# Optimization experiments

Hardware: AMD Instinct MI355X
Metric: run time of the kernel (lower is better)

Reference implementation:

```python
import jax, jax.numpy as jnp
import numpy as np

N = 50000   # nodes
E = 200000  # edges per relation
R = 4       # relations
IN = 128
HID = 32
H = 4
OUT = 32


def setup_inputs() -> dict:
    key = jax.random.key(0)
    ks = jax.random.split(key, 32)
    w = lambda k, shape: jax.random.normal(k, shape, jnp.float32) * 0.05
    inp = {
        "x": jax.random.normal(ks[0], (N, IN), jnp.float32),
        "edge_src": jax.random.randint(ks[1], (R, E), 0, N, dtype=jnp.int32),
        "edge_dst": jax.random.randint(ks[2], (R, E), 0, N, dtype=jnp.int32),
    }
    # (d_in, heads*d_out, d_out) per layer: flatten, flatten, mean-over-heads
    dims = [(IN, H * HID, HID), (H * HID, H * HID, HID), (H * HID, H * OUT, OUT)]
    i = 3
    for l, (din, dout, d) in enumerate(dims):
        inp[f"Wsrc{l}"] = w(ks[i], (R, din, dout)); i += 1
        inp[f"bsrc{l}"] = w(ks[i], (R, dout)); i += 1
        inp[f"Wdst{l}"] = w(ks[i], (R, din, dout)); i += 1
        inp[f"bdst{l}"] = w(ks[i], (R, dout)); i += 1
        inp[f"attn{l}"] = w(ks[i], (R, H, d)); i += 1
    return inp


def rel_gatv2(h, src, dst, Ws, bs, Wd, bd, att):
    """DGL GATv2Conv for one relation: gather, leaky-relu score, edge softmax, scatter-sum."""
    n = h.shape[0]
    heads, d = att.shape
    fs = (h @ Ws + bs).reshape(n, heads, d)   # [N,H,D]
    fd = (h @ Wd + bd).reshape(n, heads, d)
    e = jax.nn.leaky_relu(fs[src] + fd[dst], 0.2)        # [E,H,D]
    score = jnp.einsum('ehd,hd->eh', e, att)             # [E,H]
    # numerically stable edge softmax segmented by destination node
    m = jax.lax.stop_gradient(jax.ops.segment_max(score, dst, num_segments=n))
    m = jnp.where(jnp.isfinite(m), m, 0.0)               # zero-in-degree guard
    ex = jnp.exp(score - m[dst])
    den = jax.ops.segment_sum(ex, dst, num_segments=n)
    a = ex / jnp.maximum(den[dst], 1e-16)                # [E,H]
    return jax.ops.segment_sum(a[:, :, None] * fs[src], dst, num_segments=n)  # [N,H,D]


def gat_layer(h, edge_src, edge_dst, Ws, bs, Wd, bd, att, mean_heads):
    out = None
    for r in range(Ws.shape[0]):  # small fixed relation count; HeteroGraphConv sums
        o = rel_gatv2(h, edge_src[r], edge_dst[r], Ws[r], bs[r], Wd[r], bd[r], att[r])
        out = o if out is None else out + o
    if mean_heads:                # last_layer_flag: mean over heads
        return out.mean(axis=1)
    return out.reshape(h.shape[0], -1)  # flatten heads


def reference(x, edge_src, edge_dst,
              Wsrc0, bsrc0, Wdst0, bdst0, attn0,
              Wsrc1, bsrc1, Wdst1, bdst1, attn1,
              Wsrc2, bsrc2, Wdst2, bdst2, attn2):
    h = gat_layer(x, edge_src, edge_dst, Wsrc0, bsrc0, Wdst0, bdst0, attn0, False)
    h = gat_layer(h, edge_src, edge_dst, Wsrc1, bsrc1, Wdst1, bdst1, attn1, False)
    h = gat_layer(h, edge_src, edge_dst, Wsrc2, bsrc2, Wdst2, bdst2, attn2, True)
    return h  # [N, OUT]
```

## Files before the change

kernel.cpp:

```cpp
#include <hip/hip_runtime.h>
#include <math.h>

#define FF 128
#define G0F 1024
#define GG 2048

typedef _Float16 half2v __attribute__((ext_vector_type(2)));
typedef _Float16 f16x8  __attribute__((ext_vector_type(8)));
typedef __fp16   fp16x2 __attribute__((ext_vector_type(2)));
typedef __attribute__((ext_vector_type(4))) float f4v;

__device__ __forceinline__ half2v u2h(unsigned u) {
    union { unsigned u; half2v h; } c; c.u = u; return c.h;
}
__device__ __forceinline__ unsigned h2u(half2v h) {
    union { unsigned u; half2v h; } c; c.h = h; return c.u;
}
__device__ __forceinline__ unsigned short f2h(float f) {
    _Float16 h = (_Float16)f;
    unsigned short u; __builtin_memcpy(&u, &h, 2); return u;
}
__device__ __forceinline__ half2v pk2h(float e) {
    union { fp16x2 p; half2v h; } c;
    c.p = __builtin_amdgcn_cvt_pkrtz(e, e);
    return c.h;
}
__device__ __forceinline__ float dot2(half2v a, half2v b, float c) {
#if __has_builtin(__builtin_amdgcn_fdot2)
    union { half2v h; fp16x2 p; } ca, cb;
    ca.h = a; cb.h = b;
    return __builtin_amdgcn_fdot2(ca.p, cb.p, c, false);
#else
    return c + (float)a.x * (float)b.x + (float)a.y * (float)b.y;
#endif
}
__device__ __forceinline__ half2v shfladd_h(half2v v, int mask) {
    return v + u2h(__shfl_xor(h2u(v), mask));
}
__device__ __forceinline__ int swz16(int row, int chunk) {
    return row * 256 + (((chunk ^ row) & 15) << 4);
}


__global__ __launch_bounds__(256) void pack0(
    const float* __restrict__ W0s_, const float* __restrict__ W0d_,
    unsigned short* __restrict__ Wp,
    const float* __restrict__ a0, const float* __restrict__ a1,
    const float* __restrict__ a2, unsigned* __restrict__ attH)
{
    int b = blockIdx.x;
    const int tid = threadIdx.x;
    if (b < 512) {
        const int t = b * 256 + tid;
        const int r   = t >> 15;
        const int mat = (t >> 14) & 1;
        const int idx = t & 16383;
        const int k = idx >> 7, nn = idx & 127;
        const float* W = mat ? W0d_ : W0s_;
        const float v = W[((size_t)r * FF + k) * FF + nn];
        const int nb = nn >> 4, lo = nn & 15;
        const int ks = k >> 5, quad = (k >> 3) & 3, j = k & 7;
        const int lane = quad * 16 + lo;
        const size_t o = ((((((size_t)r * 2 + mat) * 8 + nb) * 4 + ks) * 64 + lane) * 8) + j;
        Wp[o] = f2h(v);
        return;
    }
    b -= 512;
    const int t = b * 256 + tid;
    if (t >= 768) return;
    const int l = t >> 8, rest = t & 255;
    const float* a = (l == 0) ? a0 : (l == 1) ? a1 : a2;
    const float2 v = ((const float2*)a)[rest];
    half2v h = {(_Float16)v.x, (_Float16)v.y};
    attH[t] = h2u(h);
}

__global__ __launch_bounds__(256, 4) void fused2(
    const int* __restrict__ esrc_all, const int* __restrict__ edst_all,
    int* __restrict__ rec, int* __restrict__ ovf,
    int totalE, int ne, int n, int CB,
    const float* __restrict__ x,
    const unsigned short* __restrict__ Wp,
    const float* __restrict__ bs0, const float* __restrict__ bd0,
    unsigned short* __restrict__ fs_all, unsigned short* __restrict__ fd_all,
    int nrb,
    const float* __restrict__ W1s_, const float* __restrict__ W1d_,
    const float* __restrict__ W2s_, const float* __restrict__ W2d_,
    unsigned short* __restrict__ Wp_full)
{
    __shared__ char lsA[4096];
    __shared__ char lsC[8192];

    int b = blockIdx.x;
    const int tid = threadIdx.x;
    const int L = n << 2;

    if (b < CB) {
        const int t0 = b * 1024 + tid;
        #pragma unroll
        for (int k = 0; k < 4; ++k) {
            const int i = t0 + k * 256;
            if (i < totalE) {
                const int r = i / ne;
                const int rd = r * n + edst_all[i];
                const int src = esrc_all[i];
                const int idx = atomicAdd(&rec[(size_t)rd * 16], 1);
                if (idx < 15)      rec[(size_t)rd * 16 + 1 + idx] = src;
                else if (idx < 32) ovf[(size_t)(idx - 15) * L + rd] = src;
            }
        }
        return;
    }
    b -= CB;

    if (b < G0F) {
        const int wave = tid >> 6, lane = tid & 63;
        const int r = b & 3;
        const int half = wave & 1;
        const int mat  = wave >> 1;
        const int lo = lane & 15, quad = lane >> 4;

        const unsigned short* Wr = Wp + (size_t)r * 2 * FF * FF;
        const float* bp = mat ? bd0 : bs0;
        unsigned short* fs = fs_all + (size_t)r * n * FF;
        unsigned short* fd = fd_all + (size_t)r * n * FF;

        f16x8 B[4][4];
        #pragma unroll
        for (int nbi = 0; nbi < 4; ++nbi)
            #pragma unroll
            for (int ks = 0; ks < 4; ++ks) {
                const int nb = half * 4 + nbi;
                B[nbi][ks] = *(const f16x8*)
                    &Wr[(((((size_t)mat * 8 + nb) * 4 + ks) * 64 + lane) * 8)];
            }

        float bias[4];
        #pragma unroll
        for (int nbi = 0; nbi < 4; ++nbi)
            bias[nbi] = bp[r * FF + (half * 4 + nbi) * 16 + lo];

        const int srow = tid >> 4, schunk = tid & 15;
        const int stride = G0F >> 2;
        for (int rb = b >> 2; rb < nrb; rb += stride) {
            const int row0 = rb * 16;
            {
                const float* xs = &x[(size_t)row0 * FF + tid * 8];
                const float4 p0 = *(const float4*)&xs[0];
                const float4 p1 = *(const float4*)&xs[4];
                f16x8 v;
                v[0] = (_Float16)p0.x; v[1] = (_Float16)p0.y;
                v[2] = (_Float16)p0.z; v[3] = (_Float16)p0.w;
                v[4] = (_Float16)p1.x; v[5] = (_Float16)p1.y;
                v[6] = (_Float16)p1.z; v[7] = (_Float16)p1.w;
                *(f16x8*)&lsA[swz16(srow, schunk)] = v;
            }
            __syncthreads();

            f16x8 A[4];
            #pragma unroll
            for (int ks = 0; ks < 4; ++ks)
                A[ks] = *(const f16x8*)&lsA[swz16(lo, ks * 4 + quad)];

            f4v c[4];
            #pragma unroll
            for (int nbi = 0; nbi < 4; ++nbi)
                c[nbi] = (f4v){bias[nbi], bias[nbi], bias[nbi], bias[nbi]};

            #pragma unroll
            for (int ks = 0; ks < 4; ++ks)
                #pragma unroll
                for (int nbi = 0; nbi < 4; ++nbi)
                    c[nbi] = __builtin_amdgcn_mfma_f32_16x16x32_f16(
                        A[ks], B[nbi][ks], c[nbi], 0, 0, 0);

            #pragma unroll
            for (int nbi = 0; nbi < 4; ++nbi)
                #pragma unroll
                for (int i = 0; i < 4; ++i) {
                    const int row = quad * 4 + i;
                    const int cb  = ((half * 4 + nbi) * 16 + lo) * 2;
                    *(unsigned short*)&lsC[mat * 4096 + swz16(row, cb >> 4) + (cb & 15)]
                        = f2h(c[nbi][i]);
                }
            __syncthreads();

            #pragma unroll
            for (int p = 0; p < 2; ++p) {
                const int unit = p * 256 + tid;
                const int m    = unit >> 8;
                const int row  = (unit >> 4) & 15;
                const int ch   = unit & 15;
                const uint4 d = *(const uint4*)&lsC[m * 4096 + swz16(row, ch)];
                unsigned short* out = m ? fd : fs;
                *(uint4*)&out[(size_t)(row0 + row) * FF + ch * 8] = d;
            }
            __syncthreads();
        }
        return;
    }
    b -= G0F;

    const int t = b * 256 + tid;
    if (t >= 2 * 4 * 2 * FF * FF) return;
    const int l    = 1 + (t >> 17);
    const int rest = t & 131071;
    const int r    = rest >> 15;
    const int mat  = (rest >> 14) & 1;
    const int idx  = rest & 16383;
    const int k = idx >> 7, nn = idx & 127;
    const float* W = (l == 1) ? (mat ? W1d_ : W1s_)
                              : (mat ? W2d_ : W2s_);
    const float v = W[((size_t)r * FF + k) * FF + nn];
    const int nb = nn >> 4, lo = nn & 15;
    const int ks = k >> 5, quad = (k >> 3) & 3, j = k & 7;
    const int lane = quad * 16 + lo;
    const size_t o = (((((((size_t)l * 4 + r) * 2 + mat) * 8 + nb) * 4 + ks) * 64 + lane) * 8) + j;
    Wp_full[o] = f2h(v);
}

__global__ __launch_bounds__(256, 4) void mfma_gemm(
    const unsigned short* __restrict__ hb,
    const unsigned short* __restrict__ Wp,
    const float* __restrict__ bs_all,
    const float* __restrict__ bd_all,
    unsigned short* __restrict__ fs_all,
    unsigned short* __restrict__ fd_all,
    int nrb, int n)
{
    __shared__ char lsA[4096];
    __shared__ char lsC[8192];

    const int tid = threadIdx.x;
    const int wave = tid >> 6, lane = tid & 63;
    const int r = blockIdx.x & 3;
    const int half = wave & 1;
    const int mat  = wave >> 1;
    const int lo = lane & 15, quad = lane >> 4;

    const unsigned short* Wr = Wp + (size_t)r * 2 * FF * FF;
    const float* bp = mat ? bd_all : bs_all;
    unsigned short* fs = fs_all + (size_t)r * n * FF;
    unsigned short* fd = fd_all + (size_t)r * n * FF;

    f16x8 B[4][4];
    #pragma unroll
    for (int nbi = 0; nbi < 4; ++nbi)
        #pragma unroll
        for (int ks = 0; ks < 4; ++ks) {
            const int nb = half * 4 + nbi;
            B[nbi][ks] = *(const f16x8*)
                &Wr[(((((size_t)mat * 8 + nb) * 4 + ks) * 64 + lane) * 8)];
        }

    float bias[4];
    #pragma unroll
    for (int nbi = 0; nbi < 4; ++nbi)
        bias[nbi] = bp[r * FF + (half * 4 + nbi) * 16 + lo];

    const int srow = tid >> 4, schunk = tid & 15;
    const int stride = gridDim.x >> 2;
    for (int rb = blockIdx.x >> 2; rb < nrb; rb += stride) {
        const int row0 = rb * 16;
        {
            const uint4 g = *(const uint4*)&hb[(size_t)row0 * FF + tid * 8];
            *(uint4*)&lsA[swz16(srow, schunk)] = g;
        }
        __syncthreads();

        f16x8 A[4];
        #pragma unroll
        for (int ks = 0; ks < 4; ++ks)
            A[ks] = *(const f16x8*)&lsA[swz16(lo, ks * 4 + quad)];

        f4v c[4];
        #pragma unroll
        for (int nbi = 0; nbi < 4; ++nbi)
            c[nbi] = (f4v){bias[nbi], bias[nbi], bias[nbi], bias[nbi]};

        #pragma unroll
        for (int ks = 0; ks < 4; ++ks)
            #pragma unroll
            for (int nbi = 0; nbi < 4; ++nbi)
                c[nbi] = __builtin_amdgcn_mfma_f32_16x16x32_f16(
                    A[ks], B[nbi][ks], c[nbi], 0, 0, 0);

        #pragma unroll
        for (int nbi = 0; nbi < 4; ++nbi)
            #pragma unroll
            for (int i = 0; i < 4; ++i) {
                const int row = quad * 4 + i;
                const int cb  = ((half * 4 + nbi) * 16 + lo) * 2;
                *(unsigned short*)&lsC[mat * 4096 + swz16(row, cb >> 4) + (cb & 15)]
                    = f2h(c[nbi][i]);
            }
        __syncthreads();

        #pragma unroll
        for (int p = 0; p < 2; ++p) {
            const int unit = p * 256 + tid;
            const int m    = unit >> 8;
            const int row  = (unit >> 4) & 15;
            const int ch   = unit & 15;
            const uint4 d = *(const uint4*)&lsC[m * 4096 + swz16(row, ch)];
            unsigned short* out = m ? fd : fs;
            *(uint4*)&out[(size_t)(row0 + row) * FF + ch * 8] = d;
        }
        __syncthreads();
    }
}

__device__ __forceinline__ void edge4(
    uint4 g, bool ok, const half2v* fdv, const half2v* atv,
    float& den, half2v* acc)
{
    const half2v C02 = {(_Float16)0.2f, (_Float16)0.2f};
    half2v f[4] = {u2h(g.x), u2h(g.y), u2h(g.z), u2h(g.w)};
    float v = 0.f;
    #pragma unroll
    for (int i = 0; i < 4; ++i) {
        const half2v z = f[i] + fdv[i];
        const half2v l = __builtin_elementwise_max(z, z * C02);
        v = dot2(l, atv[i], v);
    }
    v += __shfl_xor(v, 2);
    v += __shfl_xor(v, 1);
    const float e = ok ? __expf(v) : 0.f;
    den += e;
    const half2v eh = pk2h(e);
    #pragma unroll
    for (int i = 0; i < 4; ++i) acc[i] += eh * f[i];
}

__global__ __launch_bounds__(256) void aggregate(
    const int* __restrict__ rec,
    const int* __restrict__ ovf,
    const unsigned* __restrict__ fs_all,
    const unsigned* __restrict__ fd_all,
    const unsigned* __restrict__ att_h,
    unsigned* __restrict__ out_h,
    float* __restrict__ out_f32,
    int n)
{
    const int node = blockIdx.x * 4 + (threadIdx.x >> 6);
    if (node >= n) return;
    const int lane = threadIdx.x & 63;
    const int quarter = lane >> 4;
    const int q = lane & 15;
    const int fo = 4 * q;
    const int L = n << 2;

    int m[4], i0[4], i1[4];
    #pragma unroll
    for (int r = 0; r < 4; ++r) {
        const int rd = r * n + node;
        const int* rp = &rec[(size_t)rd * 16];
        m[r]  = rp[0];
        i0[r] = rp[1 + quarter];
        i1[r] = rp[5 + quarter];
    }

    half2v val[4];
    #pragma unroll
    for (int i = 0; i < 4; ++i) val[i] = (half2v){(_Float16)0.f, (_Float16)0.f};

    #pragma unroll
    for (int rp2 = 0; rp2 < 2; ++rp2) {
        const int ra = 2 * rp2, rb = 2 * rp2 + 1;
        const int rdA = ra * n + node;
        const int rdB = rb * n + node;
        const int mA = m[ra], mB = m[rb];
        const unsigned* fsuA = fs_all + (size_t)ra * n * 64;
        const unsigned* fsuB = fs_all + (size_t)rb * n * 64;

        const uint4 ufdA = *(const uint4*)&fd_all[(size_t)rdA * 64 + fo];
        const uint4 ufdB = *(const uint4*)&fd_all[(size_t)rdB * 64 + fo];
        const uint4 uatA = *(const uint4*)&att_h[ra * 64 + fo];
        const uint4 uatB = *(const uint4*)&att_h[rb * 64 + fo];

        const bool okA0 = quarter < mA, okA1 = 4 + quarter < mA;
        const bool okB0 = quarter < mB, okB1 = 4 + quarter < mB;
        int iA0 = okA0 ? i0[ra] : 0;
        int iB0 = okB0 ? i0[rb] : 0;
        int iA1 = okA1 ? i1[ra] : 0;
        int iB1 = okB1 ? i1[rb] : 0;
        const uint4 gA0 = *(const uint4*)&fsuA[(size_t)iA0 * 64 + fo];
        const uint4 gB0 = *(const uint4*)&fsuB[(size_t)iB0 * 64 + fo];
        const uint4 gA1 = *(const uint4*)&fsuA[(size_t)iA1 * 64 + fo];
        const uint4 gB1 = *(const uint4*)&fsuB[(size_t)iB1 * 64 + fo];

        half2v fdvA[4] = {u2h(ufdA.x), u2h(ufdA.y), u2h(ufdA.z), u2h(ufdA.w)};
        half2v atvA[4] = {u2h(uatA.x), u2h(uatA.y), u2h(uatA.z), u2h(uatA.w)};
        half2v fdvB[4] = {u2h(ufdB.x), u2h(ufdB.y), u2h(ufdB.z), u2h(ufdB.w)};
        half2v atvB[4] = {u2h(uatB.x), u2h(uatB.y), u2h(uatB.z), u2h(uatB.w)};

        float denA = 0.f, denB = 0.f;
        half2v accA[4], accB[4];
        #pragma unroll
        for (int i = 0; i < 4; ++i) {
            accA[i] = (half2v){(_Float16)0.f, (_Float16)0.f};
            accB[i] = (half2v){(_Float16)0.f, (_Float16)0.f};
        }

        edge4(gA0, okA0, fdvA, atvA, denA, accA);
        edge4(gB0, okB0, fdvB, atvB, denB, accB);
        if (mA > 4) edge4(gA1, okA1, fdvA, atvA, denA, accA);
        if (mB > 4) edge4(gB1, okB1, fdvB, atvB, denB, accB);

        if (mA > 8) {
            for (int p = 8; p < mA; p += 4) {
                const int ei = p + quarter;
                const bool ok = ei < mA;
                const int eic = ei < 31 ? ei : 31;
                int s = (eic < 15) ? rec[(size_t)rdA * 16 + 1 + eic]
                                   : ovf[(size_t)(eic - 15) * L + rdA];
                s = ok ? s : 0;
                const uint4 g = *(const uint4*)&fsuA[(size_t)s * 64 + fo];
                edge4(g, ok, fdvA, atvA, denA, accA);
            }
        }
        if (mB > 8) {
            for (int p = 8; p < mB; p += 4) {
                const int ei = p + quarter;
                const bool ok = ei < mB;
                const int eic = ei < 31 ? ei : 31;
                int s = (eic < 15) ? rec[(size_t)rdB * 16 + 1 + eic]
                                   : ovf[(size_t)(eic - 15) * L + rdB];
                s = ok ? s : 0;
                const uint4 g = *(const uint4*)&fsuB[(size_t)s * 64 + fo];
                edge4(g, ok, fdvB, atvB, denB, accB);
            }
        }

        if (mA) {
            denA += __shfl_xor(denA, 16);
            denA += __shfl_xor(denA, 32);
            const half2v ih = pk2h(__builtin_amdgcn_rcpf(denA));
            #pragma unroll
            for (int i = 0; i < 4; ++i) val[i] += accA[i] * ih;
        }
        if (mB) {
            denB += __shfl_xor(denB, 16);
            denB += __shfl_xor(denB, 32);
            const half2v ih = pk2h(__builtin_amdgcn_rcpf(denB));
            #pragma unroll
            for (int i = 0; i < 4; ++i) val[i] += accB[i] * ih;
        }
    }

    #pragma unroll
    for (int i = 0; i < 4; ++i) {
        val[i] = shfladd_h(val[i], 16);
        val[i] = shfladd_h(val[i], 32);
    }

    if (out_f32) {
        #pragma unroll
        for (int i = 0; i < 4; ++i) {
            val[i] = shfladd_h(val[i], 4);
            val[i] = shfladd_h(val[i], 8);
        }
        if (lane < 4) {
            float* o = &out_f32[(size_t)node * 32 + 8 * lane];
            *(float4*)&o[0] = make_float4(0.25f * (float)val[0].x, 0.25f * (float)val[0].y,
                                          0.25f * (float)val[1].x, 0.25f * (float)val[1].y);
            *(float4*)&o[4] = make_float4(0.25f * (float)val[2].x, 0.25f * (float)val[2].y,
                                          0.25f * (float)val[3].x, 0.25f * (float)val[3].y);
        }
    } else {
        if (lane < 16) {
            uint4 o;
            o.x = h2u(val[0]); o.y = h2u(val[1]);
            o.z = h2u(val[2]); o.w = h2u(val[3]);
            *(uint4*)&out_h[(size_t)node * 64 + fo] = o;
        }
    }
}

extern "C" void kernel_launch(void* const* d_in, const int* in_sizes, int n_in,
                              void* d_out, int out_size, void* d_ws, size_t ws_size,
                              hipStream_t stream)
{
    const int n  = in_sizes[0] / FF;
    const int R  = 4;
    const int ne = in_sizes[1] / R;
    const int totalE = R * ne;
    const int L  = R * n;
    const int nrb = (n + 15) / 16;

    const float* x    = (const float*)d_in[0];
    const int*   esrc = (const int*)d_in[1];
    const int*   edst = (const int*)d_in[2];

    char* p = (char*)d_ws;
    auto carve = [&p](size_t bytes) { char* q = p; p += (bytes + 255) & ~(size_t)255; return q; };
    unsigned*       hbA    = (unsigned*)      carve((size_t)n * 64 * 4);
    unsigned*       hbB    = (unsigned*)      carve((size_t)n * 64 * 4);
    unsigned short* fs_all = (unsigned short*)carve((size_t)R * n * FF * 2);
    unsigned short* fd_all = (unsigned short*)carve((size_t)R * n * FF * 2);
    unsigned short* Wp     = (unsigned short*)carve((size_t)3 * R * 2 * FF * FF * 2);
    unsigned*       attH   = (unsigned*)      carve((size_t)3 * R * 64 * 4);
    int*            rec    = (int*)           carve((size_t)L * 16 * 4);
    int*            ovf    = (int*)           carve((size_t)17 * L * 4);

    (void)hipMemsetAsync(rec, 0, (size_t)L * 16 * sizeof(int), stream);

    pack0<<<515, 256, 0, stream>>>(
        (const float*)d_in[3], (const float*)d_in[5], Wp,
        (const float*)d_in[7], (const float*)d_in[12], (const float*)d_in[17],
        attH);

    const int CB = (totalE + 1023) / 1024;
    fused2<<<CB + G0F + 1024, 256, 0, stream>>>(
        esrc, edst, rec, ovf, totalE, ne, n, CB,
        x, Wp,
        (const float*)d_in[4], (const float*)d_in[6],
        fs_all, fd_all, nrb,
        (const float*)d_in[8],  (const float*)d_in[10],
        (const float*)d_in[13], (const float*)d_in[15],
        Wp);

    unsigned* bufs[3] = {hbA, hbB, nullptr};
    for (int l = 0; l < 3; ++l) {
        if (l > 0) {
            const float* bsrc = (const float*)d_in[3 + 5 * l + 1];
            const float* bdst = (const float*)d_in[3 + 5 * l + 3];
            mfma_gemm<<<GG, 256, 0, stream>>>(
                (const unsigned short*)bufs[l - 1],
                Wp + (size_t)l * R * 2 * FF * FF,
                bsrc, bdst, fs_all, fd_all, nrb, n);
        }
        const int last = (l == 2);
        aggregate<<<(n + 3) / 4, 256, 0, stream>>>(
            rec, ovf,
            (const unsigned*)fs_all, (const unsigned*)fd_all,
            attH + (size_t)l * R * 64,
            last ? nullptr : bufs[l],
            last ? (float*)d_out : nullptr, n);
    }
}
```

Measured before the change: 376.2 us.

## Bucket edges by destination block, then build adjacency records in shared memory

```diff
diff --git a/kernel.cpp b/kernel.cpp
--- a/kernel.cpp
+++ b/kernel.cpp
@@ -4,6 +4,8 @@
 #define FF 128
 #define G0F 1024
 #define GG 2048
+#define BSH 8
+#define CAPB 256
 
 typedef _Float16 half2v __attribute__((ext_vector_type(2)));
 typedef _Float16 f16x8  __attribute__((ext_vector_type(8)));
@@ -75,10 +77,10 @@
     attH[t] = h2u(h);
 }
 
-__global__ __launch_bounds__(256, 4) void fused2(
+__global__ __launch_bounds__(256, 4) void fused3(
     const int* __restrict__ esrc_all, const int* __restrict__ edst_all,
-    int* __restrict__ rec, int* __restrict__ ovf,
-    int totalE, int ne, int n, int CB,
+    int* __restrict__ bcur, unsigned* __restrict__ bbuf,
+    int totalE, int ne, int n, int NB, int CB2,
     const float* __restrict__ x,
     const unsigned short* __restrict__ Wp,
     const float* __restrict__ bs0, const float* __restrict__ bd0,
@@ -93,9 +95,9 @@
 
     int b = blockIdx.x;
     const int tid = threadIdx.x;
-    const int L = n << 2;
-
-    if (b < CB) {
+
+    if (b < CB2) {
+        const int part = b & 7;
         const int t0 = b * 1024 + tid;
         #pragma unroll
         for (int k = 0; k < 4; ++k) {
@@ -104,14 +106,17 @@
                 const int r = i / ne;
                 const int rd = r * n + edst_all[i];
                 const int src = esrc_all[i];
-                const int idx = atomicAdd(&rec[(size_t)rd * 16], 1);
-                if (idx < 15)      rec[(size_t)rd * 16 + 1 + idx] = src;
-                else if (idx < 32) ovf[(size_t)(idx - 15) * L + rd] = src;
+                const int bkt = rd >> BSH;
+                const int reg = part * NB + bkt;
+                const int pos = atomicAdd(&bcur[reg << 4], 1);
+                if (pos < CAPB)
+                    bbuf[((size_t)reg << 8) + pos] =
+                        ((unsigned)(rd & 255) << 16) | (unsigned)src;
             }
         }
         return;
     }
-    b -= CB;
+    b -= CB2;
 
     if (b < G0F) {
         const int wave = tid >> 6, lane = tid & 63;
@@ -219,6 +224,49 @@
     Wp_full[o] = f2h(v);
 }
 
+__global__ __launch_bounds__(256) void p3build(
+    const int* __restrict__ bcur, const unsigned* __restrict__ bbuf,
+    int* __restrict__ rec, int* __restrict__ ovf, int NB, int L)
+{
+    __shared__ int lrec[256 * 17];
+    const int b = blockIdx.x;
+    const int tid = threadIdx.x;
+
+    #pragma unroll
+    for (int k = 0; k < 17; ++k) lrec[k * 256 + tid] = 0;
+    __syncthreads();
+
+    const int rd0 = b << BSH;
+    for (int part = 0; part < 8; ++part) {
+        const int reg = part * NB + b;
+        int c = bcur[reg << 4];
+        c = c < CAPB ? c : CAPB;
+        const unsigned* seg = &bbuf[(size_t)reg << 8];
+        for (int e = tid; e < c; e += 256) {
+            const unsigned v = seg[e];
+            const int rdL = v >> 16;
+            const int src = (int)(v & 0xFFFFu);
+            const int idx = atomicAdd(&lrec[rdL * 17], 1);
+            if (idx < 15)      lrec[rdL * 17 + 1 + idx] = src;
+            else if (idx < 32) ovf[(size_t)(idx - 15) * L + rd0 + rdL] = src;
+        }
+    }
+    __syncthreads();
+
+    if (rd0 + tid < L) {
+        int* out = &rec[(size_t)(rd0 + tid) * 16];
+        #pragma unroll
+        for (int w = 0; w < 4; ++w) {
+            int4 d;
+            d.x = lrec[tid * 17 + w * 4 + 0];
+            d.y = lrec[tid * 17 + w * 4 + 1];
+            d.z = lrec[tid * 17 + w * 4 + 2];
+            d.w = lrec[tid * 17 + w * 4 + 3];
+            *(int4*)&out[w * 4] = d;
+        }
+    }
+}
+
 __global__ __launch_bounds__(256, 4) void mfma_gemm(
     const unsigned short* __restrict__ hb,
     const unsigned short* __restrict__ Wp,
@@ -487,6 +535,7 @@
     const int totalE = R * ne;
     const int L  = R * n;
     const int nrb = (n + 15) / 16;
+    const int NB = (L + 255) >> BSH;
 
     const float* x    = (const float*)d_in[0];
     const int*   esrc = (const int*)d_in[1];
@@ -502,23 +551,27 @@
     unsigned*       attH   = (unsigned*)      carve((size_t)3 * R * 64 * 4);
     int*            rec    = (int*)           carve((size_t)L * 16 * 4);
     int*            ovf    = (int*)           carve((size_t)17 * L * 4);
-
-    (void)hipMemsetAsync(rec, 0, (size_t)L * 16 * sizeof(int), stream);
+    int*            bcur   = (int*)           carve((size_t)8 * NB * 16 * 4);
+    unsigned*       bbuf   = (unsigned*)      carve((size_t)8 * NB * CAPB * 4);
+
+    (void)hipMemsetAsync(bcur, 0, (size_t)8 * NB * 16 * sizeof(int), stream);
 
     pack0<<<515, 256, 0, stream>>>(
         (const float*)d_in[3], (const float*)d_in[5], Wp,
         (const float*)d_in[7], (const float*)d_in[12], (const float*)d_in[17],
         attH);
 
-    const int CB = (totalE + 1023) / 1024;
-    fused2<<<CB + G0F + 1024, 256, 0, stream>>>(
-        esrc, edst, rec, ovf, totalE, ne, n, CB,
+    const int CB2 = (totalE + 1023) / 1024;
+    fused3<<<CB2 + G0F + 1024, 256, 0, stream>>>(
+        esrc, edst, bcur, bbuf, totalE, ne, n, NB, CB2,
         x, Wp,
         (const float*)d_in[4], (const float*)d_in[6],
         fs_all, fd_all, nrb,
         (const float*)d_in[8],  (const float*)d_in[10],
         (const float*)d_in[13], (const float*)d_in[15],
         Wp);
+
+    p3build<<<NB, 256, 0, stream>>>(bcur, bbuf, rec, ovf, NB, L);
 
     unsigned* bufs[3] = {hbA, hbB, nullptr};
     for (int l = 0; l < 3; ++l) {
```

Result: no change. 377.9 us (+0.4%).

## Fuse edge aggregation with next layer's projection GEMM per 16-node tile

Applied to the files above, without the earlier changes.

```diff
diff --git a/kernel.cpp b/kernel.cpp
--- a/kernel.cpp
+++ b/kernel.cpp
@@ -3,7 +3,6 @@
 
 #define FF 128
 #define G0F 1024
-#define GG 2048
 
 typedef _Float16 half2v __attribute__((ext_vector_type(2)));
 typedef _Float16 f16x8  __attribute__((ext_vector_type(8)));
@@ -219,97 +218,6 @@
     Wp_full[o] = f2h(v);
 }
 
-__global__ __launch_bounds__(256, 4) void mfma_gemm(
-    const unsigned short* __restrict__ hb,
-    const unsigned short* __restrict__ Wp,
-    const float* __restrict__ bs_all,
-    const float* __restrict__ bd_all,
-    unsigned short* __restrict__ fs_all,
-    unsigned short* __restrict__ fd_all,
-    int nrb, int n)
-{
-    __shared__ char lsA[4096];
-    __shared__ char lsC[8192];
-
-    const int tid = threadIdx.x;
-    const int wave = tid >> 6, lane = tid & 63;
-    const int r = blockIdx.x & 3;
-    const int half = wave & 1;
-    const int mat  = wave >> 1;
-    const int lo = lane & 15, quad = lane >> 4;
-
-    const unsigned short* Wr = Wp + (size_t)r * 2 * FF * FF;
-    const float* bp = mat ? bd_all : bs_all;
-    unsigned short* fs = fs_all + (size_t)r * n * FF;
-    unsigned short* fd = fd_all + (size_t)r * n * FF;
-
-    f16x8 B[4][4];
-    #pragma unroll
-    for (int nbi = 0; nbi < 4; ++nbi)
-        #pragma unroll
-        for (int ks = 0; ks < 4; ++ks) {
-            const int nb = half * 4 + nbi;
-            B[nbi][ks] = *(const f16x8*)
-                &Wr[(((((size_t)mat * 8 + nb) * 4 + ks) * 64 + lane) * 8)];
-        }
-
-    float bias[4];
-    #pragma unroll
-    for (int nbi = 0; nbi < 4; ++nbi)
-        bias[nbi] = bp[r * FF + (half * 4 + nbi) * 16 + lo];
-
-    const int srow = tid >> 4, schunk = tid & 15;
-    const int stride = gridDim.x >> 2;
-    for (int rb = blockIdx.x >> 2; rb < nrb; rb += stride) {
-        const int row0 = rb * 16;
-        {
-            const uint4 g = *(const uint4*)&hb[(size_t)row0 * FF + tid * 8];
-            *(uint4*)&lsA[swz16(srow, schunk)] = g;
-        }
-        __syncthreads();
-
-        f16x8 A[4];
-        #pragma unroll
-        for (int ks = 0; ks < 4; ++ks)
-            A[ks] = *(const f16x8*)&lsA[swz16(lo, ks * 4 + quad)];
-
-        f4v c[4];
-        #pragma unroll
-        for (int nbi = 0; nbi < 4; ++nbi)
-            c[nbi] = (f4v){bias[nbi], bias[nbi], bias[nbi], bias[nbi]};
-
-        #pragma unroll
-        for (int ks = 0; ks < 4; ++ks)
-            #pragma unroll
-            for (int nbi = 0; nbi < 4; ++nbi)
-                c[nbi] = __builtin_amdgcn_mfma_f32_16x16x32_f16(
-                    A[ks], B[nbi][ks], c[nbi], 0, 0, 0);
-
-        #pragma unroll
-        for (int nbi = 0; nbi < 4; ++nbi)
-            #pragma unroll
-            for (int i = 0; i < 4; ++i) {
-                const int row = quad * 4 + i;
-                const int cb  = ((half * 4 + nbi) * 16 + lo) * 2;
-                *(unsigned short*)&lsC[mat * 4096 + swz16(row, cb >> 4) + (cb & 15)]
-                    = f2h(c[nbi][i]);
-            }
-        __syncthreads();
-
-        #pragma unroll
-        for (int p = 0; p < 2; ++p) {
-            const int unit = p * 256 + tid;
-            const int m    = unit >> 8;
-            const int row  = (unit >> 4) & 15;
-            const int ch   = unit & 15;
-            const uint4 d = *(const uint4*)&lsC[m * 4096 + swz16(row, ch)];
-            unsigned short* out = m ? fd : fs;
-            *(uint4*)&out[(size_t)(row0 + row) * FF + ch * 8] = d;
-        }
-        __syncthreads();
-    }
-}
-
 __device__ __forceinline__ void edge4(
     uint4 g, bool ok, const half2v* fdv, const half2v* atv,
     float& den, half2v* acc)
@@ -332,24 +240,13 @@
     for (int i = 0; i < 4; ++i) acc[i] += eh * f[i];
 }
 
-__global__ __launch_bounds__(256) void aggregate(
-    const int* __restrict__ rec,
-    const int* __restrict__ ovf,
-    const unsigned* __restrict__ fs_all,
-    const unsigned* __restrict__ fd_all,
-    const unsigned* __restrict__ att_h,
-    unsigned* __restrict__ out_h,
-    float* __restrict__ out_f32,
-    int n)
-{
-    const int node = blockIdx.x * 4 + (threadIdx.x >> 6);
-    if (node >= n) return;
-    const int lane = threadIdx.x & 63;
-    const int quarter = lane >> 4;
-    const int q = lane & 15;
-    const int fo = 4 * q;
+__device__ __forceinline__ void agg_node(
+    int node, int n, int quarter, int fo,
+    const int* __restrict__ rec, const int* __restrict__ ovf,
+    const unsigned* __restrict__ fs_all, const unsigned* __restrict__ fd_all,
+    const unsigned* __restrict__ att_h, half2v* val)
+{
     const int L = n << 2;
-
     int m[4], i0[4], i1[4];
     #pragma unroll
     for (int r = 0; r < 4; ++r) {
@@ -360,7 +257,6 @@
         i1[r] = rp[5 + quarter];
     }
 
-    half2v val[4];
     #pragma unroll
     for (int i = 0; i < 4; ++i) val[i] = (half2v){(_Float16)0.f, (_Float16)0.f};
 
@@ -453,27 +349,133 @@
         val[i] = shfladd_h(val[i], 16);
         val[i] = shfladd_h(val[i], 32);
     }
-
-    if (out_f32) {
-        #pragma unroll
-        for (int i = 0; i < 4; ++i) {
-            val[i] = shfladd_h(val[i], 4);
-            val[i] = shfladd_h(val[i], 8);
-        }
-        if (lane < 4) {
-            float* o = &out_f32[(size_t)node * 32 + 8 * lane];
-            *(float4*)&o[0] = make_float4(0.25f * (float)val[0].x, 0.25f * (float)val[0].y,
-                                          0.25f * (float)val[1].x, 0.25f * (float)val[1].y);
-            *(float4*)&o[4] = make_float4(0.25f * (float)val[2].x, 0.25f * (float)val[2].y,
-                                          0.25f * (float)val[3].x, 0.25f * (float)val[3].y);
-        }
-    } else {
+}
+
+__global__ __launch_bounds__(256) void agg_gemm(
+    const int* __restrict__ rec, const int* __restrict__ ovf,
+    const unsigned* __restrict__ fs_in, const unsigned* __restrict__ fd_in,
+    const unsigned* __restrict__ att_h,
+    const unsigned short* __restrict__ Wp,
+    const float* __restrict__ bs_nx, const float* __restrict__ bd_nx,
+    unsigned short* __restrict__ fs_out, unsigned short* __restrict__ fd_out,
+    int n)
+{
+    __shared__ char lsA[4096];
+    __shared__ char lsC[8192];
+
+    const int tid = threadIdx.x;
+    const int wave = tid >> 6, lane = tid & 63;
+    const int quarter = lane >> 4;
+    const int q = lane & 15;
+    const int fo = 4 * q;
+    const int base = blockIdx.x * 16;
+
+    for (int g = 0; g < 4; ++g) {
+        int node = base + g * 4 + wave;
+        if (node >= n) node = n - 1;
+        half2v val[4];
+        agg_node(node, n, quarter, fo, rec, ovf, fs_in, fd_in, att_h, val);
         if (lane < 16) {
             uint4 o;
             o.x = h2u(val[0]); o.y = h2u(val[1]);
             o.z = h2u(val[2]); o.w = h2u(val[3]);
-            *(uint4*)&out_h[(size_t)node * 64 + fo] = o;
-        }
+            *(uint4*)&lsA[swz16(g * 4 + wave, q)] = o;
+        }
+    }
+    __syncthreads();
+
+    const int half = wave & 1;
+    const int mat  = wave >> 1;
+    const int lo = lane & 15, quad = lane >> 4;
+
+    f16x8 A[4];
+    #pragma unroll
+    for (int ks = 0; ks < 4; ++ks)
+        A[ks] = *(const f16x8*)&lsA[swz16(lo, ks * 4 + quad)];
+
+    const float* bp = mat ? bd_nx : bs_nx;
+
+    for (int r = 0; r < 4; ++r) {
+        const unsigned short* Wr = Wp + (size_t)r * 2 * FF * FF;
+
+        f16x8 B[4][4];
+        #pragma unroll
+        for (int nbi = 0; nbi < 4; ++nbi)
+            #pragma unroll
+            for (int ks = 0; ks < 4; ++ks) {
+                const int nb = half * 4 + nbi;
+                B[nbi][ks] = *(const f16x8*)
+                    &Wr[(((((size_t)mat * 8 + nb) * 4 + ks) * 64 + lane) * 8)];
+            }
+
+        f4v c[4];
+        #pragma unroll
+        for (int nbi = 0; nbi < 4; ++nbi) {
+            const float bias = bp[r * FF + (half * 4 + nbi) * 16 + lo];
+            c[nbi] = (f4v){bias, bias, bias, bias};
+        }
+
+        #pragma unroll
+        for (int ks = 0; ks < 4; ++ks)
+            #pragma unroll
+            for (int nbi = 0; nbi < 4; ++nbi)
+                c[nbi] = __builtin_amdgcn_mfma_f32_16x16x32_f16(
+                    A[ks], B[nbi][ks], c[nbi], 0, 0, 0);
+
+        #pragma unroll
+        for (int nbi = 0; nbi < 4; ++nbi)
+            #pragma unroll
+            for (int i = 0; i < 4; ++i) {
+                const int row = quad * 4 + i;
+                const int cb  = ((half * 4 + nbi) * 16 + lo) * 2;
+                *(unsigned short*)&lsC[mat * 4096 + swz16(row, cb >> 4) + (cb & 15)]
+                    = f2h(c[nbi][i]);
+            }
+        __syncthreads();
+
+        #pragma unroll
+        for (int p = 0; p < 2; ++p) {
+            const int unit = p * 256 + tid;
+            const int m    = unit >> 8;
+            const int row  = (unit >> 4) & 15;
+            const int ch   = unit & 15;
+            if (base + row < n) {
+                const uint4 d = *(const uint4*)&lsC[m * 4096 + swz16(row, ch)];
+                unsigned short* out = (m ? fd_out : fs_out) + (size_t)r * n * FF;
+                *(uint4*)&out[(size_t)(base + row) * FF + ch * 8] = d;
+            }
+        }
+        __syncthreads();
+    }
+}
+
+__global__ __launch_bounds__(256) void aggregate(
+    const int* __restrict__ rec, const int* __restrict__ ovf,
+    const unsigned* __restrict__ fs_all, const unsigned* __restrict__ fd_all,
+    const unsigned* __restrict__ att_h,
+    float* __restrict__ out_f32, int n)
+{
+    const int node = blockIdx.x * 4 + (threadIdx.x >> 6);
+    if (node >= n) return;
+    const int lane = threadIdx.x & 63;
+    const int quarter = lane >> 4;
+    const int q = lane & 15;
+    const int fo = 4 * q;
+
+    half2v val[4];
+    agg_node(node, n, quarter, fo, rec, ovf, fs_all, fd_all, att_h, val);
+
+    #pragma unroll
+    for (int i = 0; i < 4; ++i) {
+        val[i] = shfladd_h(val[i], 4);
+        val[i] = shfladd_h(val[i], 8);
+    }
+    if (lane < 4) {
+        float* o = &out_f32[(size_t)node * 32 + 8 * lane];
+        *(float4*)&o[0] = make_float4(0.25f * (float)val[0].x, 0.25f * (float)val[0].y,
+                                      0.25f * (float)val[1].x, 0.25f * (float)val[1].y);
+        *(float4*)&o[4] = make_float4(0.25f * (float)val[2].x, 0.25f * (float)val[2].y,
+                                      0.25f * (float)val[3].x, 0.25f * (float)val[3].y);
     }
 }
 
@@ -494,14 +496,14 @@
 
     char* p = (char*)d_ws;
     auto carve = [&p](size_t bytes) { char* q = p; p += (bytes + 255) & ~(size_t)255; return q; };
-    unsigned*       hbA    = (unsigned*)      carve((size_t)n * 64 * 4);
-    unsigned*       hbB    = (unsigned*)      carve((size_t)n * 64 * 4);
-    unsigned short* fs_all = (unsigned short*)carve((size_t)R * n * FF * 2);
-    unsigned short* fd_all = (unsigned short*)carve((size_t)R * n * FF * 2);
-    unsigned short* Wp     = (unsigned short*)carve((size_t)3 * R * 2 * FF * FF * 2);
-    unsigned*       attH   = (unsigned*)      carve((size_t)3 * R * 64 * 4);
-    int*            rec    = (int*)           carve((size_t)L * 16 * 4);
-    int*            ovf    = (int*)           carve((size_t)17 * L * 4);
+    unsigned short* fsA = (unsigned short*)carve((size_t)R * n * FF * 2);
+    unsigned short* fdA = (unsigned short*)carve((size_t)R * n * FF * 2);
+    unsigned short* fsB = (unsigned short*)carve((size_t)R * n * FF * 2);
+    unsigned short* fdB = (unsigned short*)carve((size_t)R * n * FF * 2);
+    unsigned short* Wp  = (unsigned short*)carve((size_t)3 * R * 2 * FF * FF * 2);
+    unsigned*       attH= (unsigned*)      carve((size_t)3 * R * 64 * 4);
+    int*            rec = (int*)           carve((size_t)L * 16 * 4);
+    int*            ovf = (int*)           carve((size_t)17 * L * 4);
 
     (void)hipMemsetAsync(rec, 0, (size_t)L * 16 * sizeof(int), stream);
 
@@ -515,27 +517,28 @@
         esrc, edst, rec, ovf, totalE, ne, n, CB,
         x, Wp,
         (const float*)d_in[4], (const float*)d_in[6],
-        fs_all, fd_all, nrb,
+        fsA, fdA, nrb,
         (const float*)d_in[8],  (const float*)d_in[10],
         (const float*)d_in[13], (const float*)d_in[15],
         Wp);
 
-    unsigned* bufs[3] = {hbA, hbB, nullptr};
-    for (int l = 0; l < 3; ++l) {
-        if (l > 0) {
-            const float* bsrc = (const float*)d_in[3 + 5 * l + 1];
-            const float* bdst = (const float*)d_in[3 + 5 * l + 3];
-            mfma_gemm<<<GG, 256, 0, stream>>>(
-                (const unsigned short*)bufs[l - 1],
-                Wp + (size_t)l * R * 2 * FF * FF,
-                bsrc, bdst, fs_all, fd_all, nrb, n);
-        }
-        const int last = (l == 2);
-        aggregate<<<(n + 3) / 4, 256, 0, stream>>>(
-            rec, ovf,
-            (const unsigned*)fs_all, (const unsigned*)fd_all,
-            attH + (size_t)l * R * 64,
-            last ? nullptr : bufs[l],
-            last ? (float*)d_out : nullptr, n);
-    }
-}
+    const size_t sect = (size_t)R * 2 * FF * FF;
+    const int AG = (n + 15) / 16;
+
+    agg_gemm<<<AG, 256, 0, stream>>>(
+        rec, ovf, (const unsigned*)fsA, (const unsigned*)fdA,
+        attH + 0 * R * 64,
+        Wp + 1 * sect, (const float*)d_in[9], (const float*)d_in[11],
+        fsB, fdB, n);
+
+    agg_gemm<<<AG, 256, 0, stream>>>(
+        rec, ovf, (const unsigned*)fsB, (const unsigned*)fdB,
+        attH + 1 * R * 64,
+        Wp + 2 * sect, (const float*)d_in[14], (const float*)d_in[16],
+        fsA, fdA, n);
+
+    aggregate<<<(n + 3) / 4, 256, 0, stream>>>(
+        rec, ovf, (const unsigned*)fsA, (const unsigned*)fdA,
+        attH + 2 * R * 64,
+        (float*)d_out, n);
+}
```

New measurement: 410.6 us. 9.1% more time.
